# Kernel optimization log

Measured on AMD Instinct MI355X. Metric: run time of the kernel, lower is better.

The kernel has to match this reference:

```python
import jax, jax.numpy as jnp
import numpy as np

K_SPARSE = 128

# NOTE: F.dropout(x, 0.02) in the source defaults to training=True; it is omitted
# here (identity) so the reference is deterministic for kernel correctness checks.
# sparsify2 (from matching-pursuit modules/sparse.py) flattens to (B, C*T), takes
# top-k, and returns: sparse reconstruction (B,C,T), amplitude-scaled channel
# one-hots (B,k,C), and time one-hots (B,k,T).

def setup_inputs() -> dict:
    key = jax.random.key(0)
    ks = jax.random.split(key, 5)
    B, C, H, T = 16, 1024, 4096, 512
    x = jax.random.normal(ks[0], (B, C, T), dtype=jnp.float32)
    up_w = jax.random.normal(ks[1], (H, C), dtype=jnp.float32) * (1.0 / np.sqrt(C))
    up_b = jax.random.normal(ks[2], (H,), dtype=jnp.float32) * 0.01
    sal_w = jax.random.normal(ks[3], (H, C), dtype=jnp.float32) * (1.0 / np.sqrt(C))
    sal_b = jax.random.normal(ks[4], (H,), dtype=jnp.float32) * 0.01
    return {"x": x, "up_w": up_w, "up_b": up_b, "sal_w": sal_w, "sal_b": sal_b}


def reference(x, up_w, up_b, sal_w, sal_b):
    B, C, T = x.shape
    H = up_w.shape[0]
    # 1x1 convs == per-timestep matmuls
    sig = jnp.einsum('bct,hc->bht', x, up_w) + up_b[None, :, None]
    sal = jnp.einsum('bct,hc->bht', x, sal_w) + sal_b[None, :, None]
    # global softmax over flattened (hidden*time) per batch item
    sal = jax.nn.softmax(sal.reshape(B, H * T), axis=-1).reshape(B, H, T)
    y = sig * sal  # (B, H, T)

    flat = y.reshape(B, H * T)
    values, indices = jax.lax.top_k(flat, K_SPARSE)  # (B, k)

    # sparse reconstruction: zeros everywhere except top-k entries
    brows = jnp.arange(B)[:, None]
    sparse = jnp.zeros_like(flat).at[brows, indices].set(values).reshape(B, H, T)

    ch_idx = indices // T   # (B, k) channel of each kept atom
    t_idx = indices % T     # (B, k) time of each kept atom
    packed = jax.nn.one_hot(ch_idx, H, dtype=y.dtype) * values[..., None]  # (B, k, H)
    time_oh = jax.nn.one_hot(t_idx, T, dtype=y.dtype)                       # (B, k, T)
    return sparse, packed, time_oh
```

## Files before the change

### kernel.cpp

```cpp
#include <hip/hip_runtime.h>
#include <stdint.h>

#define B_    16
#define C_    1024
#define H_    4096
#define T_    512
#define HT    (H_*T_)
#define KSP   128
#define NBINS 4096
#define KEY_LO   (-8.0f)
#define KEY_INVW (204.8f)
#define MARGIN   64
#define CAP      4096

typedef __bf16 bf16x8 __attribute__((ext_vector_type(8)));
typedef float  f32x4  __attribute__((ext_vector_type(4)));

static __device__ __forceinline__ unsigned short f2bf(float f) {
  union { float f; uint32_t u; } v; v.f = f;
  uint32_t u = v.u;
  return (unsigned short)((u + 0x7FFFu + ((u >> 16) & 1u)) >> 16);
}
static __device__ __forceinline__ float bf2f(unsigned short s) {
  union { uint32_t u; float f; } v; v.u = ((uint32_t)s) << 16;
  return v.f;
}
static __device__ __forceinline__ int key_bin(float kf) {
  float b = (kf - KEY_LO) * KEY_INVW;
  b = fminf(fmaxf(b, 0.0f), 4095.0f);
  return (int)b;
}
static __device__ __forceinline__ void async_load16(const void* g, void* l) {
  __builtin_amdgcn_global_load_lds((const __attribute__((address_space(1))) void*)g,
                                   (__attribute__((address_space(3))) void*)l, 16, 0, 0);
}
static __device__ __forceinline__ unsigned long long d2u(double d) {
  union { double d; unsigned long long u; } v; v.d = d;
  unsigned long long u = v.u;
  return (u >> 63) ? ~u : (u | 0x8000000000000000ull);
}
static __device__ __forceinline__ double u2d(unsigned long long s) {
  union { unsigned long long u; double d; } v;
  v.u = (s >> 63) ? (s & 0x7FFFFFFFFFFFFFFFull) : ~s;
  return v.d;
}

__global__ void k_conv_w(const float* __restrict__ srcA, unsigned short* __restrict__ dstA,
                         const float* __restrict__ srcB, unsigned short* __restrict__ dstB,
                         int n4) {
  int i = blockIdx.x * 256 + threadIdx.x;
  const float* src; unsigned short* dst; int j;
  if (i < n4) { src = srcA; dst = dstA; j = i; }
  else if (i < 2 * n4) { src = srcB; dst = dstB; j = i - n4; }
  else return;
  float4 v = ((const float4*)src)[j];
  ushort4 o; o.x = f2bf(v.x); o.y = f2bf(v.y); o.z = f2bf(v.z); o.w = f2bf(v.w);
  ((ushort4*)dst)[j] = o;
}

__global__ void k_transpose_x(const float* __restrict__ x, float* __restrict__ xT32,
                              unsigned short* __restrict__ xT16) {
  int b  = blockIdx.z;
  int t0 = blockIdx.x * 64;
  int c0 = blockIdx.y * 64;
  __shared__ float tile[64][65];
  int tt = threadIdx.x & 63;
  int g  = threadIdx.x >> 6;
  const float* xb = x + (size_t)b * C_ * T_;
  #pragma unroll
  for (int it = 0; it < 16; ++it) {
    int cl = g + it * 4;
    tile[cl][tt] = xb[(size_t)(c0 + cl) * T_ + t0 + tt];
  }
  __syncthreads();
  float* oT = xT32 + (size_t)b * T_ * C_;
  unsigned short* oH = xT16 + (size_t)b * T_ * C_;
  #pragma unroll
  for (int it = 0; it < 16; ++it) {
    int tl = g + it * 4;
    float v = tile[tt][tl];
    oT[(size_t)(t0 + tl) * C_ + c0 + tt] = v;
    oH[(size_t)(t0 + tl) * C_ + c0 + tt] = f2bf(v);
  }
}

__launch_bounds__(256, 2)
__global__ void k_gemm(const unsigned short* __restrict__ wup16,
                       const unsigned short* __restrict__ wsal16,
                       const unsigned short* __restrict__ xT16,
                       const float* __restrict__ up_b,
                       const float* __restrict__ sal_b,
                       unsigned char* __restrict__ keys8,
                       float2* __restrict__ partials,
                       unsigned int* __restrict__ ghist) {
  int b     = blockIdx.y;
  int tileH = blockIdx.x >> 2;
  int tileT = blockIdx.x & 3;
  int tid  = threadIdx.x;
  int lane = tid & 63, wave = tid >> 6;
  int waveR = wave >> 1, waveC = wave & 1;

  __shared__ __align__(16) char smem[49152];
  __shared__ float redA[4], redB[4];
  char* sA = smem;
  char* sS = smem + 16384;
  char* sB = smem + 32768;

  f32x4 accU[4][4], accS[4][4];
  #pragma unroll
  for (int m = 0; m < 4; ++m)
    #pragma unroll
    for (int n = 0; n < 4; ++n) { accU[m][n] = (f32x4){0,0,0,0}; accS[m][n] = (f32x4){0,0,0,0}; }

  int srcChunk = (lane & 7) ^ (lane >> 3);
  const unsigned short* gA[4]; const unsigned short* gS[4]; const unsigned short* gB[4];
  #pragma unroll
  for (int j = 0; j < 4; ++j) {
    int r = j * 32 + wave * 8 + (lane >> 3);
    gA[j] = wup16  + (size_t)(tileH * 128 + r) * C_ + srcChunk * 8;
    gS[j] = wsal16 + (size_t)(tileH * 128 + r) * C_ + srcChunk * 8;
    gB[j] = xT16   + (size_t)b * T_ * C_ + (size_t)(tileT * 128 + r) * C_ + srcChunk * 8;
  }
  int rowL = lane & 15;
  int fragChunk = (lane >> 4) * 16;
  int swz = (lane & 7) << 4;

  for (int step = 0; step < 16; ++step) {
    int k0 = step * 64;
    #pragma unroll
    for (int j = 0; j < 4; ++j) {
      char* la = sA + j * 4096 + wave * 1024;
      char* ls = sS + j * 4096 + wave * 1024;
      char* lb = sB + j * 4096 + wave * 1024;
      async_load16(gA[j] + k0, la);
      async_load16(gS[j] + k0, ls);
      async_load16(gB[j] + k0, lb);
    }
    __syncthreads();
    #pragma unroll
    for (int ksub = 0; ksub < 2; ++ksub) {
      int kb = ksub * 64 + fragChunk;
      bf16x8 bf[4];
      #pragma unroll
      for (int n = 0; n < 4; ++n) {
        int row = waveC * 64 + n * 16 + rowL;
        bf[n] = *(const bf16x8*)(sB + row * 128 + (kb ^ swz));
      }
      #pragma unroll
      for (int m = 0; m < 4; ++m) {
        int row = waveR * 64 + m * 16 + rowL;
        bf16x8 au = *(const bf16x8*)(sA + row * 128 + (kb ^ swz));
        bf16x8 as = *(const bf16x8*)(sS + row * 128 + (kb ^ swz));
        #pragma unroll
        for (int n = 0; n < 4; ++n) {
          accU[m][n] = __builtin_amdgcn_mfma_f32_16x16x32_bf16(au, bf[n], accU[m][n], 0, 0, 0);
          accS[m][n] = __builtin_amdgcn_mfma_f32_16x16x32_bf16(as, bf[n], accS[m][n], 0, 0, 0);
        }
      }
    }
    __syncthreads();
  }

  int hb = tileH * 128 + waveR * 64;
  int tb = tileT * 128 + waveC * 64;
  int colL  = lane & 15;
  int rowHi = (lane >> 4) * 4;
  #pragma unroll
  for (int m = 0; m < 4; ++m)
    #pragma unroll
    for (int r = 0; r < 4; ++r) {
      int h = hb + m * 16 + rowHi + r;
      float ub = up_b[h], sb = sal_b[h];
      #pragma unroll
      for (int n = 0; n < 4; ++n) { accU[m][n][r] += ub; accS[m][n][r] += sb; }
    }

  float lm = -INFINITY;
  #pragma unroll
  for (int m = 0; m < 4; ++m)
    #pragma unroll
    for (int n = 0; n < 4; ++n)
      #pragma unroll
      for (int r = 0; r < 4; ++r) lm = fmaxf(lm, accS[m][n][r]);
  for (int o = 32; o; o >>= 1) lm = fmaxf(lm, __shfl_xor(lm, o));
  if (lane == 0) redA[wave] = lm;
  __syncthreads();
  float M = fmaxf(fmaxf(redA[0], redA[1]), fmaxf(redA[2], redA[3]));
  float ls = 0.0f;
  #pragma unroll
  for (int m = 0; m < 4; ++m)
    #pragma unroll
    for (int n = 0; n < 4; ++n)
      #pragma unroll
      for (int r = 0; r < 4; ++r) ls += __expf(accS[m][n][r] - M);
  for (int o = 32; o; o >>= 1) ls += __shfl_xor(ls, o);
  if (lane == 0) redB[wave] = ls;
  __syncthreads();
  if (tid == 0)
    partials[b * 128 + blockIdx.x] = make_float2(M, redB[0] + redB[1] + redB[2] + redB[3]);

  unsigned int* hist = (unsigned int*)smem;
  for (int i = tid; i < NBINS; i += 256) hist[i] = 0;
  __syncthreads();
  unsigned char* keysB = keys8 + (size_t)b * HT;
  #pragma unroll
  for (int m = 0; m < 4; ++m)
    #pragma unroll
    for (int n = 0; n < 4; ++n)
      #pragma unroll
      for (int r = 0; r < 4; ++r) {
        float sig = accU[m][n][r];
        float sal = accS[m][n][r];
        float key = (sig > 0.0f) ? (__logf(sig) + sal) : -INFINITY;
        unsigned short kb16 = f2bf(key);
        int bin = key_bin(bf2f(kb16));
        int h = hb + m * 16 + rowHi + r;
        int t = tb + n * 16 + colL;
        keysB[(size_t)h * T_ + t] = (unsigned char)(bin >> 4);
        atomicAdd(&hist[bin], 1u);
      }
  __syncthreads();
  unsigned int* gh = ghist + b * NBINS;
  for (int i = tid; i < NBINS; i += 256) {
    unsigned int cv = hist[i];
    if (cv) atomicAdd(&gh[i], cv);
  }
}

__global__ void k_reduce(const float2* __restrict__ partials,
                         const unsigned int* __restrict__ ghist,
                         float* __restrict__ Mv, float* __restrict__ Sv,
                         int* __restrict__ thetaBin) {
  int b = blockIdx.x; int tid = threadIdx.x; int lane = tid & 63;
  __shared__ float sm[128], ss[128];
  __shared__ unsigned int hloc[NBINS];
  __shared__ unsigned int segsum[256];
  __shared__ float redM[2], redS[2];
  if (tid < 128) { float2 p = partials[b * 128 + tid]; sm[tid] = p.x; ss[tid] = p.y; }
  const unsigned int* gh = ghist + b * NBINS;
  int hi = 4095 - 16 * tid;
  unsigned int seg = 0;
  #pragma unroll
  for (int k = 0; k < 16; ++k) { unsigned int c = gh[hi - k]; hloc[hi - k] = c; seg += c; }
  segsum[tid] = seg;
  __syncthreads();
  if (tid < 128) {
    float m = sm[tid];
    for (int o = 32; o; o >>= 1) m = fmaxf(m, __shfl_xor(m, o));
    if (lane == 0) redM[tid >> 6] = m;
  }
  __syncthreads();
  float M = fmaxf(redM[0], redM[1]);
  if (tid < 128) {
    float s = ss[tid] * __expf(sm[tid] - M);
    for (int o = 32; o; o >>= 1) s += __shfl_xor(s, o);
    if (lane == 0) redS[tid >> 6] = s;
  }
  __syncthreads();
  if (tid == 0) {
    Mv[b] = M; Sv[b] = redS[0] + redS[1];
    unsigned int acc = 0; int theta = 1; int sidx = 0;
    while (sidx < 256 && acc + segsum[sidx] < KSP) { acc += segsum[sidx]; ++sidx; }
    if (sidx < 256) {
      int h2 = 4095 - 16 * sidx;
      for (int k = 0; k < 16; ++k) {
        acc += hloc[h2 - k];
        if (acc >= KSP) { theta = h2 - k; break; }
      }
    }
    theta -= MARGIN; if (theta < 1) theta = 1;
    thetaBin[b] = theta;
  }
}

__global__ void k_collect(const unsigned char* __restrict__ keys8,
                          const int* __restrict__ thetaBin,
                          unsigned int* __restrict__ cnt,
                          unsigned int* __restrict__ cand) {
  __shared__ unsigned int wtot[4], wbase[4];
  int tid = threadIdx.x;
  int lane = tid & 63, wave = tid >> 6;
  size_t blockBase = (size_t)blockIdx.x * 8192;
  int b = (int)(blockBase >> 21);
  unsigned int localBase = (unsigned int)(blockBase & (HT - 1));
  unsigned int thetaU8 = (unsigned int)(thetaBin[b] >> 4);
  const unsigned char* kb = keys8 + blockBase;

  uint4 v[2];
  #pragma unroll
  for (int j = 0; j < 2; ++j) v[j] = *(const uint4*)(kb + j * 4096 + tid * 16);

  unsigned int mask = 0, mycnt = 0;
  #pragma unroll
  for (int j = 0; j < 2; ++j) {
    unsigned int ww[4] = {v[j].x, v[j].y, v[j].z, v[j].w};
    #pragma unroll
    for (int q = 0; q < 4; ++q) {
      #pragma unroll
      for (int k = 0; k < 4; ++k) {
        unsigned int bv = (ww[q] >> (8 * k)) & 0xFFu;
        if (bv >= thetaU8) { mask |= 1u << (j * 16 + q * 4 + k); ++mycnt; }
      }
    }
  }

  unsigned int pre = mycnt;
  #pragma unroll
  for (int o = 1; o < 64; o <<= 1) {
    unsigned int t = __shfl_up(pre, o);
    if (lane >= o) pre += t;
  }
  unsigned int myExcl = pre - mycnt;
  if (lane == 63) wtot[wave] = pre;
  __syncthreads();
  if (tid == 0) {
    unsigned int tot = wtot[0] + wtot[1] + wtot[2] + wtot[3];
    unsigned int gbase = tot ? atomicAdd(&cnt[b], tot) : 0u;
    unsigned int acc = gbase;
    #pragma unroll
    for (int w = 0; w < 4; ++w) { wbase[w] = acc; acc += wtot[w]; }
  }
  __syncthreads();
  unsigned int pos = wbase[wave] + myExcl;
  unsigned int m = mask;
  while (m) {
    int i = __ffs(m) - 1; m &= m - 1;
    int j = i >> 4, rq = i & 15;
    unsigned int idx = localBase + (unsigned int)(j * 4096 + tid * 16 + rq);
    if (pos < CAP) cand[b * CAP + pos] = idx;
    ++pos;
  }
}

__global__ void k_refine(const float* __restrict__ xT32, const float* __restrict__ wup,
                         const float* __restrict__ wsal, const float* __restrict__ up_b,
                         const float* __restrict__ sal_b, const unsigned int* __restrict__ cnt,
                         const unsigned int* __restrict__ cand, double* __restrict__ keyd) {
  int b = blockIdx.y;
  unsigned int nc = cnt[b];
  int n = nc < CAP ? (int)nc : CAP;
  int lane = threadIdx.x & 63;
  int wid = blockIdx.x * 4 + (threadIdx.x >> 6);
  for (int slot = wid; slot < n; slot += 512) {
    unsigned int idx = cand[b * CAP + slot];
    int h = (int)(idx >> 9), t = (int)(idx & 511);
    const float4* wv = (const float4*)(wup  + (size_t)h * C_);
    const float4* sv = (const float4*)(wsal + (size_t)h * C_);
    const float4* xv = (const float4*)(xT32 + ((size_t)b * T_ + t) * C_);
    double du = 0.0, ds = 0.0;
    #pragma unroll
    for (int j = 0; j < 4; ++j) {
      float4 w4 = wv[lane + 64 * j];
      float4 s4 = sv[lane + 64 * j];
      float4 x4 = xv[lane + 64 * j];
      du += (double)w4.x * x4.x + (double)w4.y * x4.y + (double)w4.z * x4.z + (double)w4.w * x4.w;
      ds += (double)s4.x * x4.x + (double)s4.y * x4.y + (double)s4.z * x4.z + (double)s4.w * x4.w;
    }
    #pragma unroll
    for (int o = 32; o; o >>= 1) { du += __shfl_xor(du, o); ds += __shfl_xor(ds, o); }
    if (lane == 0) {
      double sig = du + (double)up_b[h];
      double sal = ds + (double)sal_b[h];
      keyd[b * CAP + slot] = (sig > 0.0) ? (log(sig) + sal) : -1e300;
    }
  }
}

__launch_bounds__(256, 1)
__global__ void k_final(const double* __restrict__ keyd, const unsigned int* __restrict__ cnt,
                        const unsigned int* __restrict__ cand, const float* __restrict__ Mv,
                        const float* __restrict__ Sv, float* __restrict__ out) {
  int b = blockIdx.x; int tid = threadIdx.x;
  unsigned int nc = cnt[b];
  int n = nc < CAP ? (int)nc : CAP;
  int L = 256;
  while (L < n) L <<= 1;

  __shared__ unsigned long long sk[CAP];
  __shared__ unsigned int sid[CAP];
  for (int i = tid; i < L; i += 256) {
    if (i < n) { sk[i] = ~d2u(keyd[b * CAP + i]); sid[i] = cand[b * CAP + i]; }
    else       { sk[i] = 0xFFFFFFFFFFFFFFFFull;   sid[i] = 0xFFFFFFFFu; }
  }
  for (int size = 2; size <= L; size <<= 1) {
    for (int stride = size >> 1; stride > 0; stride >>= 1) {
      __syncthreads();
      for (int i = tid; i < (L >> 1); i += 256) {
        int ix = 2 * i - (i & (stride - 1));
        int iy = ix + stride;
        bool asc = ((ix & size) == 0);
        unsigned long long ka = sk[ix], kb = sk[iy];
        unsigned int ia = sid[ix], ib = sid[iy];
        bool aLessB = (ka < kb) || (ka == kb && ia < ib);
        if (asc != aLessB) { sk[ix] = kb; sk[iy] = ka; sid[ix] = ib; sid[iy] = ia; }
      }
    }
  }
  __syncthreads();
  if (tid < KSP) {
    unsigned int idx = sid[tid];
    if (idx != 0xFFFFFFFFu) {
      double key = u2d(~sk[tid]);
      double val = exp(key - (double)Mv[b]) / (double)Sv[b];
      float vf = (float)val;
      int h = (int)(idx >> 9), t = (int)(idx & 511);
      out[(size_t)b * HT + idx] = vf;
      out[(size_t)B_ * HT + ((size_t)b * KSP + tid) * H_ + h] = vf;
      out[(size_t)B_ * HT + (size_t)B_ * KSP * H_ + ((size_t)b * KSP + tid) * T_ + t] = 1.0f;
    }
  }
}

extern "C" void kernel_launch(void* const* d_in, const int* in_sizes, int n_in,
                              void* d_out, int out_size, void* d_ws, size_t ws_size,
                              hipStream_t stream) {
  const float* x    = (const float*)d_in[0];
  const float* wup  = (const float*)d_in[1];
  const float* upb  = (const float*)d_in[2];
  const float* wsal = (const float*)d_in[3];
  const float* salb = (const float*)d_in[4];
  float* out = (float*)d_out;

  char* ob = (char*)d_out;
  unsigned char*  keys8  = (unsigned char*)(ob);
  float*          xT32   = (float*)(ob + 33554432);
  unsigned short* xT16   = (unsigned short*)(ob + 67108864);
  unsigned short* wup16  = (unsigned short*)(ob + 83886080);
  unsigned short* wsal16 = (unsigned short*)(ob + 92274688);

  char* wb = (char*)d_ws;
  unsigned int* ghist  = (unsigned int*)wb;
  unsigned int* cnt    = (unsigned int*)(wb + 262144);
  int*          thetaB = (int*)(wb + 262208);
  float*        Mv     = (float*)(wb + 262272);
  float*        Sv     = (float*)(wb + 262336);
  float2*       parts  = (float2*)(wb + 262400);
  unsigned int* cand   = (unsigned int*)(wb + 278784);
  double*       keyd   = (double*)(wb + 540928);

  hipMemsetAsync(d_ws, 0, 262208, stream);
  k_conv_w<<<8192, 256, 0, stream>>>(wup, wup16, wsal, wsal16, (H_ * C_) / 4);
  k_transpose_x<<<dim3(T_ / 64, C_ / 64, B_), 256, 0, stream>>>(x, xT32, xT16);
  k_gemm<<<dim3(128, B_), 256, 0, stream>>>(wup16, wsal16, xT16, upb, salb, keys8, parts, ghist);
  k_reduce<<<B_, 256, 0, stream>>>(parts, ghist, Mv, Sv, thetaB);
  k_collect<<<4096, 256, 0, stream>>>(keys8, thetaB, cnt, cand);
  k_refine<<<dim3(128, B_), 256, 0, stream>>>(xT32, wup, wsal, upb, salb, cnt, cand, keyd);
  hipMemsetAsync(d_out, 0, (size_t)out_size * 4, stream);
  k_final<<<B_, 256, 0, stream>>>(keyd, cnt, cand, Mv, Sv, out);
}
```

Measured before the change: 315.1 us.

## Double-buffer GEMM LDS with phased MFMA/load interleave and larger 128x256 tiles

Reworks the dual-GEMM kernel to use 512-thread blocks covering 128x256 output tiles, so each B tile load is shared by twice as many outputs. Shared memory is double-buffered at 128KB, and each K step is split into four phases that issue the async global-to-LDS loads for the next step while MFMAs run on the current buffer, with explicit barriers, setprio and sched_barrier to control ordering. The reduce kernel is adjusted to the halved number of partials. The large LDS footprint limits occupancy to one block per CU, and the hand-placed barriers and waitcnts add risk of subtle ordering bugs.

```diff
diff --git a/kernel.cpp b/kernel.cpp
--- a/kernel.cpp
+++ b/kernel.cpp
@@ -44,6 +44,12 @@
   v.u = (s >> 63) ? (s & 0x7FFFFFFFFFFFFFFFull) : ~s;
   return v.d;
 }
+static __device__ __forceinline__ bf16x8 ldfrag(const char* base, int row, int kb, int swz) {
+  return *(const bf16x8*)(base + row * 128 + (kb ^ swz));
+}
+#define MFMA(a, b, c) __builtin_amdgcn_mfma_f32_16x16x32_bf16(a, b, c, 0, 0, 0)
+#define VMDRAIN asm volatile("s_waitcnt vmcnt(0)" ::: "memory")
+#define NOFIN ((void)0)
 
 __global__ void k_conv_w(const float* __restrict__ srcA, unsigned short* __restrict__ dstA,
                          const float* __restrict__ srcB, unsigned short* __restrict__ dstB,
@@ -84,7 +90,46 @@
   }
 }
 
-__launch_bounds__(256, 2)
+#define PHASE(CB, KB, M0, M1, LOADBF, FIN, ...)                                 \
+  do {                                                                          \
+    if (LOADBF) {                                                               \
+      bfv0 = ldfrag((CB) + 32768, rB +  0, (KB), swz);                          \
+      bfv1 = ldfrag((CB) + 32768, rB + 16, (KB), swz);                          \
+      bfv2 = ldfrag((CB) + 32768, rB + 32, (KB), swz);                          \
+      bfv3 = ldfrag((CB) + 32768, rB + 48, (KB), swz);                          \
+    }                                                                           \
+    bf16x8 aU0 = ldfrag((CB),         rA + (M0) * 16, (KB), swz);               \
+    bf16x8 aS0 = ldfrag((CB) + 16384, rA + (M0) * 16, (KB), swz);               \
+    bf16x8 aU1 = ldfrag((CB),         rA + (M1) * 16, (KB), swz);               \
+    bf16x8 aS1 = ldfrag((CB) + 16384, rA + (M1) * 16, (KB), swz);               \
+    __VA_ARGS__;                                                                \
+    __builtin_amdgcn_s_barrier();                                               \
+    asm volatile("s_waitcnt lgkmcnt(0)" ::: "memory");                          \
+    __builtin_amdgcn_sched_barrier(0);                                          \
+    __builtin_amdgcn_s_setprio(1);                                              \
+    accU[M0][0] = MFMA(aU0, bfv0, accU[M0][0]);                                 \
+    accU[M0][1] = MFMA(aU0, bfv1, accU[M0][1]);                                 \
+    accU[M0][2] = MFMA(aU0, bfv2, accU[M0][2]);                                 \
+    accU[M0][3] = MFMA(aU0, bfv3, accU[M0][3]);                                 \
+    accS[M0][0] = MFMA(aS0, bfv0, accS[M0][0]);                                 \
+    accS[M0][1] = MFMA(aS0, bfv1, accS[M0][1]);                                 \
+    accS[M0][2] = MFMA(aS0, bfv2, accS[M0][2]);                                 \
+    accS[M0][3] = MFMA(aS0, bfv3, accS[M0][3]);                                 \
+    accU[M1][0] = MFMA(aU1, bfv0, accU[M1][0]);                                 \
+    accU[M1][1] = MFMA(aU1, bfv1, accU[M1][1]);                                 \
+    accU[M1][2] = MFMA(aU1, bfv2, accU[M1][2]);                                 \
+    accU[M1][3] = MFMA(aU1, bfv3, accU[M1][3]);                                 \
+    accS[M1][0] = MFMA(aS1, bfv0, accS[M1][0]);                                 \
+    accS[M1][1] = MFMA(aS1, bfv1, accS[M1][1]);                                 \
+    accS[M1][2] = MFMA(aS1, bfv2, accS[M1][2]);                                 \
+    accS[M1][3] = MFMA(aS1, bfv3, accS[M1][3]);                                 \
+    __builtin_amdgcn_s_setprio(0);                                              \
+    __builtin_amdgcn_sched_barrier(0);                                          \
+    FIN;                                                                        \
+    __builtin_amdgcn_s_barrier();                                               \
+  } while (0)
+
+__launch_bounds__(512, 2)
 __global__ void k_gemm(const unsigned short* __restrict__ wup16,
                        const unsigned short* __restrict__ wsal16,
                        const unsigned short* __restrict__ xT16,
@@ -94,17 +139,14 @@
                        float2* __restrict__ partials,
                        unsigned int* __restrict__ ghist) {
   int b     = blockIdx.y;
-  int tileH = blockIdx.x >> 2;
-  int tileT = blockIdx.x & 3;
+  int tileH = blockIdx.x >> 1;
+  int tileT = blockIdx.x & 1;
   int tid  = threadIdx.x;
   int lane = tid & 63, wave = tid >> 6;
-  int waveR = wave >> 1, waveC = wave & 1;
-
-  __shared__ __align__(16) char smem[49152];
-  __shared__ float redA[4], redB[4];
-  char* sA = smem;
-  char* sS = smem + 16384;
-  char* sB = smem + 32768;
+  int waveR = wave >> 2, waveC = wave & 3;
+
+  __shared__ __align__(16) char smem[131072];
+  __shared__ float redA[8], redB[8];
 
   f32x4 accU[4][4], accS[4][4];
   #pragma unroll
@@ -112,57 +154,64 @@
     #pragma unroll
     for (int n = 0; n < 4; ++n) { accU[m][n] = (f32x4){0,0,0,0}; accS[m][n] = (f32x4){0,0,0,0}; }
 
-  int srcChunk = (lane & 7) ^ (lane >> 3);
-  const unsigned short* gA[4]; const unsigned short* gS[4]; const unsigned short* gB[4];
-  #pragma unroll
-  for (int j = 0; j < 4; ++j) {
-    int r = j * 32 + wave * 8 + (lane >> 3);
-    gA[j] = wup16  + (size_t)(tileH * 128 + r) * C_ + srcChunk * 8;
-    gS[j] = wsal16 + (size_t)(tileH * 128 + r) * C_ + srcChunk * 8;
-    gB[j] = xT16   + (size_t)b * T_ * C_ + (size_t)(tileT * 128 + r) * C_ + srcChunk * 8;
-  }
+  int rgrp = tid >> 3;
+  int srcChunk = (tid & 7) ^ (rgrp & 7);
+  const unsigned short* gAu = wup16  + (size_t)(tileH * 128 + rgrp) * C_ + srcChunk * 8;
+  const unsigned short* gAs = wsal16 + (size_t)(tileH * 128 + rgrp) * C_ + srcChunk * 8;
+  const unsigned short* gB  = xT16 + ((size_t)b * T_ + tileT * 256 + rgrp) * C_ + srcChunk * 8;
+
   int rowL = lane & 15;
   int fragChunk = (lane >> 4) * 16;
   int swz = (lane & 7) << 4;
-
-  for (int step = 0; step < 16; ++step) {
-    int k0 = step * 64;
-    #pragma unroll
-    for (int j = 0; j < 4; ++j) {
-      char* la = sA + j * 4096 + wave * 1024;
-      char* ls = sS + j * 4096 + wave * 1024;
-      char* lb = sB + j * 4096 + wave * 1024;
-      async_load16(gA[j] + k0, la);
-      async_load16(gS[j] + k0, ls);
-      async_load16(gB[j] + k0, lb);
-    }
-    __syncthreads();
-    #pragma unroll
-    for (int ksub = 0; ksub < 2; ++ksub) {
-      int kb = ksub * 64 + fragChunk;
-      bf16x8 bf[4];
-      #pragma unroll
-      for (int n = 0; n < 4; ++n) {
-        int row = waveC * 64 + n * 16 + rowL;
-        bf[n] = *(const bf16x8*)(sB + row * 128 + (kb ^ swz));
-      }
-      #pragma unroll
-      for (int m = 0; m < 4; ++m) {
-        int row = waveR * 64 + m * 16 + rowL;
-        bf16x8 au = *(const bf16x8*)(sA + row * 128 + (kb ^ swz));
-        bf16x8 as = *(const bf16x8*)(sS + row * 128 + (kb ^ swz));
-        #pragma unroll
-        for (int n = 0; n < 4; ++n) {
-          accU[m][n] = __builtin_amdgcn_mfma_f32_16x16x32_bf16(au, bf[n], accU[m][n], 0, 0, 0);
-          accS[m][n] = __builtin_amdgcn_mfma_f32_16x16x32_bf16(as, bf[n], accS[m][n], 0, 0, 0);
-        }
-      }
-    }
-    __syncthreads();
+  int rA = waveR * 64 + rowL;
+  int rB = waveC * 64 + rowL;
+
+  bf16x8 bfv0, bfv1, bfv2, bfv3;
+
+  {
+    char* sb = smem + tid * 16;
+    async_load16(gB,            sb + 32768);
+    async_load16(gB +  64 * C_, sb + 40960);
+    async_load16(gB + 128 * C_, sb + 49152);
+    async_load16(gB + 192 * C_, sb + 57344);
+    async_load16(gAu,           sb);
+    async_load16(gAu + 64 * C_, sb + 8192);
+    async_load16(gAs,           sb + 16384);
+    async_load16(gAs + 64 * C_, sb + 24576);
+    VMDRAIN;
+    __builtin_amdgcn_s_barrier();
+  }
+
+  #pragma unroll 1
+  for (int t = 0; t < 15; ++t) {
+    char* cb = smem + (t & 1) * 65536;
+    char* sb = smem + ((t & 1) ^ 1) * 65536 + tid * 16;
+    const unsigned short* srcB = gB  + (t + 1) * 64;
+    const unsigned short* srcU = gAu + (t + 1) * 64;
+    const unsigned short* srcS = gAs + (t + 1) * 64;
+    PHASE(cb, fragChunk, 0, 1, true, NOFIN,
+          async_load16(srcB,            sb + 32768);
+          async_load16(srcB +  64 * C_, sb + 40960);
+          async_load16(srcB + 128 * C_, sb + 49152);
+          async_load16(srcB + 192 * C_, sb + 57344));
+    PHASE(cb, fragChunk, 2, 3, false, NOFIN,
+          async_load16(srcU,           sb);
+          async_load16(srcU + 64 * C_, sb + 8192);
+          async_load16(srcS,           sb + 16384);
+          async_load16(srcS + 64 * C_, sb + 24576));
+    PHASE(cb, 64 + fragChunk, 0, 1, true, NOFIN, NOFIN);
+    PHASE(cb, 64 + fragChunk, 2, 3, false, VMDRAIN, NOFIN);
+  }
+  {
+    char* cb = smem + 65536;
+    PHASE(cb, fragChunk,      0, 1, true,  NOFIN, NOFIN);
+    PHASE(cb, fragChunk,      2, 3, false, NOFIN, NOFIN);
+    PHASE(cb, 64 + fragChunk, 0, 1, true,  NOFIN, NOFIN);
+    PHASE(cb, 64 + fragChunk, 2, 3, false, NOFIN, NOFIN);
   }
 
   int hb = tileH * 128 + waveR * 64;
-  int tb = tileT * 128 + waveC * 64;
+  int tb = tileT * 256 + waveC * 64;
   int colL  = lane & 15;
   int rowHi = (lane >> 4) * 4;
   #pragma unroll
@@ -170,9 +219,9 @@
     #pragma unroll
     for (int r = 0; r < 4; ++r) {
       int h = hb + m * 16 + rowHi + r;
-      float ub = up_b[h], sb = sal_b[h];
+      float ub = up_b[h], sb2 = sal_b[h];
       #pragma unroll
-      for (int n = 0; n < 4; ++n) { accU[m][n][r] += ub; accS[m][n][r] += sb; }
+      for (int n = 0; n < 4; ++n) { accU[m][n][r] += ub; accS[m][n][r] += sb2; }
     }
 
   float lm = -INFINITY;
@@ -185,7 +234,9 @@
   for (int o = 32; o; o >>= 1) lm = fmaxf(lm, __shfl_xor(lm, o));
   if (lane == 0) redA[wave] = lm;
   __syncthreads();
-  float M = fmaxf(fmaxf(redA[0], redA[1]), fmaxf(redA[2], redA[3]));
+  float M = redA[0];
+  #pragma unroll
+  for (int w = 1; w < 8; ++w) M = fmaxf(M, redA[w]);
   float ls = 0.0f;
   #pragma unroll
   for (int m = 0; m < 4; ++m)
@@ -196,11 +247,15 @@
   for (int o = 32; o; o >>= 1) ls += __shfl_xor(ls, o);
   if (lane == 0) redB[wave] = ls;
   __syncthreads();
-  if (tid == 0)
-    partials[b * 128 + blockIdx.x] = make_float2(M, redB[0] + redB[1] + redB[2] + redB[3]);
+  if (tid == 0) {
+    float s = 0.0f;
+    #pragma unroll
+    for (int w = 0; w < 8; ++w) s += redB[w];
+    partials[b * 64 + blockIdx.x] = make_float2(M, s);
+  }
 
   unsigned int* hist = (unsigned int*)smem;
-  for (int i = tid; i < NBINS; i += 256) hist[i] = 0;
+  for (int i = tid; i < NBINS; i += 512) hist[i] = 0;
   __syncthreads();
   unsigned char* keysB = keys8 + (size_t)b * HT;
   #pragma unroll
@@ -221,7 +276,7 @@
       }
   __syncthreads();
   unsigned int* gh = ghist + b * NBINS;
-  for (int i = tid; i < NBINS; i += 256) {
+  for (int i = tid; i < NBINS; i += 512) {
     unsigned int cv = hist[i];
     if (cv) atomicAdd(&gh[i], cv);
   }
@@ -231,12 +286,12 @@
                          const unsigned int* __restrict__ ghist,
                          float* __restrict__ Mv, float* __restrict__ Sv,
                          int* __restrict__ thetaBin) {
-  int b = blockIdx.x; int tid = threadIdx.x; int lane = tid & 63;
-  __shared__ float sm[128], ss[128];
+  int b = blockIdx.x; int tid = threadIdx.x;
+  __shared__ float sm[64], ss[64];
   __shared__ unsigned int hloc[NBINS];
   __shared__ unsigned int segsum[256];
-  __shared__ float redM[2], redS[2];
-  if (tid < 128) { float2 p = partials[b * 128 + tid]; sm[tid] = p.x; ss[tid] = p.y; }
+  __shared__ float redM[1], redS[1];
+  if (tid < 64) { float2 p = partials[b * 64 + tid]; sm[tid] = p.x; ss[tid] = p.y; }
   const unsigned int* gh = ghist + b * NBINS;
   int hi = 4095 - 16 * tid;
   unsigned int seg = 0;
@@ -244,21 +299,21 @@
   for (int k = 0; k < 16; ++k) { unsigned int c = gh[hi - k]; hloc[hi - k] = c; seg += c; }
   segsum[tid] = seg;
   __syncthreads();
-  if (tid < 128) {
+  if (tid < 64) {
     float m = sm[tid];
     for (int o = 32; o; o >>= 1) m = fmaxf(m, __shfl_xor(m, o));
-    if (lane == 0) redM[tid >> 6] = m;
-  }
-  __syncthreads();
-  float M = fmaxf(redM[0], redM[1]);
-  if (tid < 128) {
+    if (tid == 0) redM[0] = m;
+  }
+  __syncthreads();
+  float M = redM[0];
+  if (tid < 64) {
     float s = ss[tid] * __expf(sm[tid] - M);
     for (int o = 32; o; o >>= 1) s += __shfl_xor(s, o);
-    if (lane == 0) redS[tid >> 6] = s;
+    if (tid == 0) redS[0] = s;
   }
   __syncthreads();
   if (tid == 0) {
-    Mv[b] = M; Sv[b] = redS[0] + redS[1];
+    Mv[b] = M; Sv[b] = redS[0];
     unsigned int acc = 0; int theta = 1; int sidx = 0;
     while (sidx < 256 && acc + segsum[sidx] < KSP) { acc += segsum[sidx]; ++sidx; }
     if (sidx < 256) {
@@ -441,7 +496,7 @@
   hipMemsetAsync(d_ws, 0, 262208, stream);
   k_conv_w<<<8192, 256, 0, stream>>>(wup, wup16, wsal, wsal16, (H_ * C_) / 4);
   k_transpose_x<<<dim3(T_ / 64, C_ / 64, B_), 256, 0, stream>>>(x, xT32, xT16);
-  k_gemm<<<dim3(128, B_), 256, 0, stream>>>(wup16, wsal16, xT16, upb, salb, keys8, parts, ghist);
+  k_gemm<<<dim3(64, B_), 512, 0, stream>>>(wup16, wsal16, xT16, upb, salb, keys8, parts, ghist);
   k_reduce<<<B_, 256, 0, stream>>>(parts, ghist, Mv, Sv, thetaB);
   k_collect<<<4096, 256, 0, stream>>>(keys8, thetaB, cnt, cand);
   k_refine<<<dim3(128, B_), 256, 0, stream>>>(xT32, wup, wsal, upb, salb, cnt, cand, keyd);
```

Measured after the change: 326.4 us. 1.04x slower.

## Fuse preprocessing kernels and overlap output zeroing with the GEMM main loop

Applied to the files above, without the earlier changes.

Merges weight conversion, x transpose, and workspace histogram zeroing into one launch, removing two launches and a memset. When the workspace is large enough, scratch buffers move out of the output buffer into the workspace. Each GEMM block then zeroes its slice of the output inside its K loop, so the separate output memset disappears and its writes hide behind compute. This adds extra store traffic in the GEMM loop and makes the layout depend on ws_size.

```diff
diff --git a/kernel.cpp b/kernel.cpp
--- a/kernel.cpp
+++ b/kernel.cpp
@@ -12,6 +12,7 @@
 #define KEY_INVW (204.8f)
 #define MARGIN   64
 #define CAP      4096
+#define ZQ    5248
 
 typedef __bf16 bf16x8 __attribute__((ext_vector_type(8)));
 typedef float  f32x4  __attribute__((ext_vector_type(4)));
@@ -45,43 +46,51 @@
   return v.d;
 }
 
-__global__ void k_conv_w(const float* __restrict__ srcA, unsigned short* __restrict__ dstA,
-                         const float* __restrict__ srcB, unsigned short* __restrict__ dstB,
-                         int n4) {
-  int i = blockIdx.x * 256 + threadIdx.x;
-  const float* src; unsigned short* dst; int j;
-  if (i < n4) { src = srcA; dst = dstA; j = i; }
-  else if (i < 2 * n4) { src = srcB; dst = dstB; j = i - n4; }
-  else return;
-  float4 v = ((const float4*)src)[j];
-  ushort4 o; o.x = f2bf(v.x); o.y = f2bf(v.y); o.z = f2bf(v.z); o.w = f2bf(v.w);
-  ((ushort4*)dst)[j] = o;
-}
-
-__global__ void k_transpose_x(const float* __restrict__ x, float* __restrict__ xT32,
-                              unsigned short* __restrict__ xT16) {
-  int b  = blockIdx.z;
-  int t0 = blockIdx.x * 64;
-  int c0 = blockIdx.y * 64;
+__global__ void k_pre(const float* __restrict__ x, const float* __restrict__ wup,
+                      const float* __restrict__ wsal,
+                      unsigned short* __restrict__ wup16, unsigned short* __restrict__ wsal16,
+                      float* __restrict__ xT32, unsigned short* __restrict__ xT16,
+                      unsigned int* __restrict__ gzero) {
+  int bid = blockIdx.x; int tid = threadIdx.x;
   __shared__ float tile[64][65];
-  int tt = threadIdx.x & 63;
-  int g  = threadIdx.x >> 6;
-  const float* xb = x + (size_t)b * C_ * T_;
-  #pragma unroll
-  for (int it = 0; it < 16; ++it) {
-    int cl = g + it * 4;
-    tile[cl][tt] = xb[(size_t)(c0 + cl) * T_ + t0 + tt];
-  }
-  __syncthreads();
-  float* oT = xT32 + (size_t)b * T_ * C_;
-  unsigned short* oH = xT16 + (size_t)b * T_ * C_;
-  #pragma unroll
-  for (int it = 0; it < 16; ++it) {
-    int tl = g + it * 4;
-    float v = tile[tt][tl];
-    oT[(size_t)(t0 + tl) * C_ + c0 + tt] = v;
-    oH[(size_t)(t0 + tl) * C_ + c0 + tt] = f2bf(v);
-  }
+  if (bid < 8192) {
+    int i = bid * 256 + tid;
+    int n4 = (H_ * C_) / 4;
+    const float* src; unsigned short* dst; int j;
+    if (i < n4) { src = wup; dst = wup16; j = i; }
+    else        { src = wsal; dst = wsal16; j = i - n4; }
+    float4 v = ((const float4*)src)[j];
+    ushort4 o; o.x = f2bf(v.x); o.y = f2bf(v.y); o.z = f2bf(v.z); o.w = f2bf(v.w);
+    ((ushort4*)dst)[j] = o;
+    return;
+  }
+  if (bid < 8192 + 2048) {
+    int r  = bid - 8192;
+    int b  = r >> 7;
+    int c0 = ((r >> 3) & 15) * 64;
+    int t0 = (r & 7) * 64;
+    int tt = tid & 63;
+    int g  = tid >> 6;
+    const float* xb = x + (size_t)b * C_ * T_;
+    #pragma unroll
+    for (int it = 0; it < 16; ++it) {
+      int cl = g + it * 4;
+      tile[cl][tt] = xb[(size_t)(c0 + cl) * T_ + t0 + tt];
+    }
+    __syncthreads();
+    float* oT = xT32 + (size_t)b * T_ * C_;
+    unsigned short* oH = xT16 + (size_t)b * T_ * C_;
+    #pragma unroll
+    for (int it = 0; it < 16; ++it) {
+      int tl = g + it * 4;
+      float v = tile[tt][tl];
+      oT[(size_t)(t0 + tl) * C_ + c0 + tt] = v;
+      oH[(size_t)(t0 + tl) * C_ + c0 + tt] = f2bf(v);
+    }
+    return;
+  }
+  int w = (bid - 10240) * 256 + tid;
+  if (w < 65552) gzero[w] = 0;
 }
 
 __launch_bounds__(256, 2)
@@ -92,7 +101,8 @@
                        const float* __restrict__ sal_b,
                        unsigned char* __restrict__ keys8,
                        float2* __restrict__ partials,
-                       unsigned int* __restrict__ ghist) {
+                       unsigned int* __restrict__ ghist,
+                       float4* __restrict__ zb_all) {
   int b     = blockIdx.y;
   int tileH = blockIdx.x >> 2;
   int tileT = blockIdx.x & 3;
@@ -105,6 +115,9 @@
   char* sA = smem;
   char* sS = smem + 16384;
   char* sB = smem + 32768;
+
+  float4* zb = zb_all ? (zb_all + (size_t)(b * 128 + blockIdx.x) * ZQ) : (float4*)0;
+  const float4 z4 = make_float4(0.f, 0.f, 0.f, 0.f);
 
   f32x4 accU[4][4], accS[4][4];
   #pragma unroll
@@ -135,6 +148,14 @@
       async_load16(gA[j] + k0, la);
       async_load16(gS[j] + k0, ls);
       async_load16(gB[j] + k0, lb);
+    }
+    if (zb) {
+      if (step < 10) {
+        zb[step * 512 + tid] = z4;
+        zb[step * 512 + 256 + tid] = z4;
+      } else if (step == 10 && tid < 128) {
+        zb[5120 + tid] = z4;
+      }
     }
     __syncthreads();
     #pragma unroll
@@ -421,13 +442,6 @@
   const float* salb = (const float*)d_in[4];
   float* out = (float*)d_out;
 
-  char* ob = (char*)d_out;
-  unsigned char*  keys8  = (unsigned char*)(ob);
-  float*          xT32   = (float*)(ob + 33554432);
-  unsigned short* xT16   = (unsigned short*)(ob + 67108864);
-  unsigned short* wup16  = (unsigned short*)(ob + 83886080);
-  unsigned short* wsal16 = (unsigned short*)(ob + 92274688);
-
   char* wb = (char*)d_ws;
   unsigned int* ghist  = (unsigned int*)wb;
   unsigned int* cnt    = (unsigned int*)(wb + 262144);
@@ -438,13 +452,23 @@
   unsigned int* cand   = (unsigned int*)(wb + 278784);
   double*       keyd   = (double*)(wb + 540928);
 
-  hipMemsetAsync(d_ws, 0, 262208, stream);
-  k_conv_w<<<8192, 256, 0, stream>>>(wup, wup16, wsal, wsal16, (H_ * C_) / 4);
-  k_transpose_x<<<dim3(T_ / 64, C_ / 64, B_), 256, 0, stream>>>(x, xT32, xT16);
-  k_gemm<<<dim3(128, B_), 256, 0, stream>>>(wup16, wsal16, xT16, upb, salb, keys8, parts, ghist);
+  const size_t SMALL_END = 1065216;
+  const size_t BIG_BYTES = 100663296;
+  bool wsPath = (ws_size >= SMALL_END + BIG_BYTES);
+  char* big = wsPath ? (wb + SMALL_END) : (char*)d_out;
+
+  unsigned char*  keys8  = (unsigned char*)(big);
+  float*          xT32   = (float*)(big + 33554432);
+  unsigned short* xT16   = (unsigned short*)(big + 67108864);
+  unsigned short* wup16  = (unsigned short*)(big + 83886080);
+  unsigned short* wsal16 = (unsigned short*)(big + 92274688);
+
+  k_pre<<<10497, 256, 0, stream>>>(x, wup, wsal, wup16, wsal16, xT32, xT16, ghist);
+  k_gemm<<<dim3(128, B_), 256, 0, stream>>>(wup16, wsal16, xT16, upb, salb, keys8, parts, ghist,
+                                            wsPath ? (float4*)d_out : (float4*)0);
   k_reduce<<<B_, 256, 0, stream>>>(parts, ghist, Mv, Sv, thetaB);
   k_collect<<<4096, 256, 0, stream>>>(keys8, thetaB, cnt, cand);
   k_refine<<<dim3(128, B_), 256, 0, stream>>>(xT32, wup, wsal, upb, salb, cnt, cand, keyd);
-  hipMemsetAsync(d_out, 0, (size_t)out_size * 4, stream);
+  if (!wsPath) hipMemsetAsync(d_out, 0, (size_t)out_size * 4, stream);
   k_final<<<B_, 256, 0, stream>>>(keyd, cnt, cand, Mv, Sv, out);
 }
```

Measured after the change: 301.3 us. -4.4%, faster.
